# Kernel optimization log

Measured on AMD Instinct MI355X. Metric: run time of the kernel, lower is better.

Reference implementation:

```python
import jax, jax.numpy as jnp
import numpy as np

B, S, DIN, DOUT, A, T, H = 8, 1024, 1024, 1024, 4, 4, 8  # arity A, T cell types, hidden H


def setup_inputs() -> dict:
    key = jax.random.key(0)
    ks = jax.random.split(key, 6)
    x = jax.random.normal(ks[0], (B, S, DIN), jnp.float32)
    sc = 1.0 / np.sqrt(DIN).astype(np.float32)
    weight = jax.random.uniform(ks[1], (A * DOUT, DIN), jnp.float32, -sc, sc)
    bias = jax.random.uniform(ks[2], (A * DOUT,), jnp.float32, -sc, sc)
    # stacked per-cell-type MLP params: arity -> H -> 1 (tanh)
    cw1 = jax.random.normal(ks[3], (T, A, H), jnp.float32) / np.sqrt(A).astype(np.float32)
    cb1 = jnp.zeros((T, H), jnp.float32)
    cw2 = jax.random.normal(ks[4], (T, H), jnp.float32) / np.sqrt(H).astype(np.float32)
    cb2 = jnp.zeros((T,), jnp.float32)
    return {"x": x, "weight": weight, "bias": bias,
            "cw1": cw1, "cb1": cb1, "cw2": cw2, "cb2": cb2}


def reference(x, weight, bias, cw1, cb1, cw2, cb2):
    T_, A_, H_ = cw1.shape
    Dout = weight.shape[0] // A_
    G = Dout // T_  # neurons per cell type (cell_indices = contiguous blocks via np.repeat)
    # all_inputs = F.linear(input, weight, bias): (B, S, A*Dout)
    z = jnp.einsum('bsd,od->bso', x, weight) + bias
    # slice per-neuron arity chunks -> (B, S, T, G, A)
    z = z.reshape(z.shape[0], z.shape[1], T_, G, A_)
    # per-cell-type MLP applied to every neuron of that type (replaces Python loop)
    h = jnp.tanh(jnp.einsum('bstga,tah->bstgh', z, cw1) + cb1[:, None, :])
    o = jnp.einsum('bstgh,th->bstg', h, cw2) + cb2[:, None]
    # concat over neurons -> (B, S, Dout)
    return o.reshape(o.shape[0], o.shape[1], Dout)
```

## Files before the change

### kernel.cpp

```cpp
#include <hip/hip_runtime.h>


typedef __bf16 bf16x8 __attribute__((ext_vector_type(8)));
typedef float f32x4 __attribute__((ext_vector_type(4)));
typedef float f32x16 __attribute__((ext_vector_type(16)));

#define BM 128
#define BN 128
#define BK 32
#define KDIM 1024
#define NITER (KDIM / BK)
#define ABUF_E (BM * BK)
#define BUF_E ((BM + BN) * BK)
#define BUF_BYTES (BUF_E * 2)
#define XN8 (8192 * 1024 / 8)
#define WN8 (4096 * 1024 / 8)

__global__ __launch_bounds__(256) void cvt_bf16_kernel(
    const float* __restrict__ x, const float* __restrict__ w,
    __bf16* __restrict__ xb, __bf16* __restrict__ wb) {
    int i = blockIdx.x * 256 + threadIdx.x;
    const float* src;
    __bf16* dst;
    int j;
    if (i < XN8) { src = x; dst = xb; j = i; }
    else         { src = w; dst = wb; j = i - XN8; }
    const f32x4* p = (const f32x4*)src + 2 * (size_t)j;
    f32x4 a = p[0], b = p[1];
    bf16x8 o;
    o[0] = (__bf16)a[0]; o[1] = (__bf16)a[1]; o[2] = (__bf16)a[2]; o[3] = (__bf16)a[3];
    o[4] = (__bf16)b[0]; o[5] = (__bf16)b[1]; o[6] = (__bf16)b[2]; o[7] = (__bf16)b[3];
    ((bf16x8*)dst)[j] = o;
}

union __align__(16) SmemU {
    __bf16 stg[2 * BUF_E];
    float  z[64 * 128];
};

__global__ __launch_bounds__(256, 4) void fused_gemm_mlp_kernel(
    const __bf16* __restrict__ Ag,
    const __bf16* __restrict__ Bg,
    const float* __restrict__ bias,
    const float* __restrict__ cw1,
    const float* __restrict__ cb1,
    const float* __restrict__ cw2,
    const float* __restrict__ cb2,
    float* __restrict__ out)
{
    __shared__ SmemU u;

    const int tid  = threadIdx.x;
    const int wave = tid >> 6;
    const int lane = tid & 63;
    const int wm = wave >> 1;
    const int wn = wave & 1;
    const int bn0 = blockIdx.x * BN;
    const int bm0 = blockIdx.y * BM;

    f32x16 acc[2][2] = {};

    const int srow4 = lane >> 2;
    const int g8    = (((lane & 3) ^ ((lane >> 3) & 3)) * 8);

    const int lr5 = lane & 31;
    const int lk2 = lane >> 5;
    const int sw2 = (lr5 >> 1) & 3;
    const int arow = (wm * 64 + lr5) * (BK * 2);
    const int brow = ABUF_E * 2 + (wn * 64 + lr5) * (BK * 2);
    int cxo[2];
#pragma unroll
    for (int kh = 0; kh < 2; ++kh)
        cxo[kh] = ((kh * 2 + lk2) ^ sw2) * 16;
    const char* sb = (const char*)u.stg;

    const __bf16* aBase = Ag + (size_t)(bm0 + (wave * 2) * 16 + srow4) * KDIM + g8;
    const __bf16* bBase = Bg + (size_t)(bn0 + (wave * 2) * 16 + srow4) * KDIM + g8;

    auto stage = [&](int it, int buf) {
        __bf16* dstA = u.stg + buf * BUF_E;
        __bf16* dstB = dstA + ABUF_E;
        const int kof = it * BK;
#pragma unroll
        for (int c = 0; c < 2; ++c) {
            const int chunk = wave * 2 + c;
            __builtin_amdgcn_global_load_lds(
                (__attribute__((address_space(1))) void*)(aBase + (size_t)c * 16 * KDIM + kof),
                (__attribute__((address_space(3))) void*)&dstA[chunk * 512],
                16, 0, 0);
            __builtin_amdgcn_global_load_lds(
                (__attribute__((address_space(1))) void*)(bBase + (size_t)c * 16 * KDIM + kof),
                (__attribute__((address_space(3))) void*)&dstB[chunk * 512],
                16, 0, 0);
        }
    };

    stage(0, 0);
    for (int it = 0; it < NITER; ++it) {
        __syncthreads();
        if (it + 1 < NITER) stage(it + 1, (it + 1) & 1);
        const char* base = sb + (it & 1) * BUF_BYTES;
#pragma unroll
        for (int kh = 0; kh < 2; ++kh) {
            bf16x8 af[2], bfr[2];
#pragma unroll
            for (int mi = 0; mi < 2; ++mi)
                af[mi] = *(const bf16x8*)(base + arow + mi * 2048 + cxo[kh]);
#pragma unroll
            for (int ni = 0; ni < 2; ++ni)
                bfr[ni] = *(const bf16x8*)(base + brow + ni * 2048 + cxo[kh]);
#pragma unroll
            for (int mi = 0; mi < 2; ++mi)
#pragma unroll
                for (int ni = 0; ni < 2; ++ni)
                    acc[mi][ni] = __builtin_amdgcn_mfma_f32_32x32x16_bf16(
                        af[mi], bfr[ni], acc[mi][ni], 0, 0, 0);
        }
    }
    __syncthreads();

    const int t = bn0 >> 10;
    const float L2E2 = 2.885390081777927f;
    float oinit = cb2[t];
#pragma unroll
    for (int i = 0; i < 8; ++i) oinit += cw2[t * 8 + i];

    float bcol[2];
#pragma unroll
    for (int ni = 0; ni < 2; ++ni)
        bcol[ni] = bias[bn0 + wn * 64 + ni * 32 + lr5];

#pragma unroll
    for (int h = 0; h < 2; ++h) {
        if (wm == h) {
#pragma unroll
            for (int mi = 0; mi < 2; ++mi) {
#pragma unroll
                for (int ni = 0; ni < 2; ++ni) {
                    const int n  = wn * 64 + ni * 32 + lr5;
                    const int gc = n >> 2;
                    const int a  = n & 3;
#pragma unroll
                    for (int g = 0; g < 4; ++g) {
                        const int rb = mi * 32 + g * 8 + lk2 * 4;
#pragma unroll
                        for (int j = 0; j < 4; ++j) {
                            const int chunk = (gc + j) & 31;
                            u.z[(rb + j) * 128 + chunk * 4 + a] =
                                acc[mi][ni][g * 4 + j] + bcol[ni];
                        }
                    }
                }
            }
        }
        __syncthreads();

#pragma unroll
        for (int it2 = 0; it2 < 8; ++it2) {
            const int i = tid + it2 * 256;
            const int q = (i & 7) + 8 * ((i >> 8) & 3);
            const int r = ((i >> 3) & 31) + 32 * (i >> 10);
            const int chunk = (q + (r & 3)) & 31;
            f32x4 z = *(const f32x4*)&u.z[r * 128 + chunk * 4];
            float o = oinit;
#pragma unroll
            for (int hh = 0; hh < 8; ++hh) {
                float pre = z[0] * cw1[t * 32 + 0 * 8 + hh] + z[1] * cw1[t * 32 + 1 * 8 + hh]
                          + z[2] * cw1[t * 32 + 2 * 8 + hh] + z[3] * cw1[t * 32 + 3 * 8 + hh]
                          + cb1[t * 8 + hh];
                float e = __builtin_amdgcn_exp2f(pre * L2E2);
                o -= 2.0f * cw2[t * 8 + hh] * __builtin_amdgcn_rcpf(e + 1.0f);
            }
            out[(size_t)(bm0 + h * 64 + r) * 1024 + (bn0 >> 2) + q] = o;
        }
        __syncthreads();
    }
}

extern "C" void kernel_launch(void* const* d_in, const int* in_sizes, int n_in,
                              void* d_out, int out_size, void* d_ws, size_t ws_size,
                              hipStream_t stream) {
    const float* x    = (const float*)d_in[0];
    const float* w    = (const float*)d_in[1];
    const float* bias = (const float*)d_in[2];
    const float* cw1  = (const float*)d_in[3];
    const float* cb1  = (const float*)d_in[4];
    const float* cw2  = (const float*)d_in[5];
    const float* cb2  = (const float*)d_in[6];
    float* out = (float*)d_out;

    __bf16* xb = (__bf16*)d_ws;
    __bf16* wb = xb + (size_t)8192 * 1024;

    cvt_bf16_kernel<<<(XN8 + WN8) / 256, 256, 0, stream>>>(x, w, xb, wb);

    dim3 grid(4096 / BN, 8192 / BM);
    fused_gemm_mlp_kernel<<<grid, 256, 0, stream>>>(xb, wb, bias, cw1, cb1, cw2, cb2, out);
}
```

Before: 200.9 us.

## Pack weight into MFMA-fragment layout and load B directly to registers

The conversion kernel now writes the bf16 weight in a k8-major packed layout, so each lane can load its B fragment straight from global memory into registers. This bypasses LDS staging for B. Only A is staged through LDS, and the main loop is unrolled by two with explicit register double-buffering of B. The __launch_bounds__ occupancy hint of 4 is dropped. B now comes from global/L2 with no LDS reuse, which may raise global traffic and latency exposure, and register pressure goes up with the two B buffers.

```diff
diff --git a/kernel.cpp b/kernel.cpp
--- a/kernel.cpp
+++ b/kernel.cpp
@@ -9,38 +9,44 @@
 #define BN 128
 #define BK 32
 #define KDIM 1024
+#define NDIM 4096
 #define NITER (KDIM / BK)
-#define ABUF_E (BM * BK)
-#define BUF_E ((BM + BN) * BK)
-#define BUF_BYTES (BUF_E * 2)
+#define ABUF_B 8192
 #define XN8 (8192 * 1024 / 8)
 #define WN8 (4096 * 1024 / 8)
 
-__global__ __launch_bounds__(256) void cvt_bf16_kernel(
+__global__ __launch_bounds__(256) void cvt_pack_kernel(
     const float* __restrict__ x, const float* __restrict__ w,
-    __bf16* __restrict__ xb, __bf16* __restrict__ wb) {
+    __bf16* __restrict__ xb, __bf16* __restrict__ wbp) {
     int i = blockIdx.x * 256 + threadIdx.x;
-    const float* src;
-    __bf16* dst;
-    int j;
-    if (i < XN8) { src = x; dst = xb; j = i; }
-    else         { src = w; dst = wb; j = i - XN8; }
-    const f32x4* p = (const f32x4*)src + 2 * (size_t)j;
-    f32x4 a = p[0], b = p[1];
-    bf16x8 o;
-    o[0] = (__bf16)a[0]; o[1] = (__bf16)a[1]; o[2] = (__bf16)a[2]; o[3] = (__bf16)a[3];
-    o[4] = (__bf16)b[0]; o[5] = (__bf16)b[1]; o[6] = (__bf16)b[2]; o[7] = (__bf16)b[3];
-    ((bf16x8*)dst)[j] = o;
+    if (i < XN8) {
+        const f32x4* p = (const f32x4*)x + 2 * (size_t)i;
+        f32x4 a = p[0], b = p[1];
+        bf16x8 o;
+        o[0]=(__bf16)a[0]; o[1]=(__bf16)a[1]; o[2]=(__bf16)a[2]; o[3]=(__bf16)a[3];
+        o[4]=(__bf16)b[0]; o[5]=(__bf16)b[1]; o[6]=(__bf16)b[2]; o[7]=(__bf16)b[3];
+        ((bf16x8*)xb)[i] = o;
+    } else {
+        const int j  = i - XN8;
+        const int n  = j >> 7;
+        const int k8 = j & 127;
+        const f32x4* p = (const f32x4*)(w + (size_t)n * KDIM + k8 * 8);
+        f32x4 a = p[0], b = p[1];
+        bf16x8 o;
+        o[0]=(__bf16)a[0]; o[1]=(__bf16)a[1]; o[2]=(__bf16)a[2]; o[3]=(__bf16)a[3];
+        o[4]=(__bf16)b[0]; o[5]=(__bf16)b[1]; o[6]=(__bf16)b[2]; o[7]=(__bf16)b[3];
+        ((bf16x8*)wbp)[(size_t)k8 * NDIM + n] = o;
+    }
 }
 
 union __align__(16) SmemU {
-    __bf16 stg[2 * BUF_E];
+    __bf16 stg[2 * (ABUF_B / 2)];
     float  z[64 * 128];
 };
 
-__global__ __launch_bounds__(256, 4) void fused_gemm_mlp_kernel(
+__global__ __launch_bounds__(256) void fused_gemm_mlp_kernel(
     const __bf16* __restrict__ Ag,
-    const __bf16* __restrict__ Bg,
+    const __bf16* __restrict__ Bw,
     const float* __restrict__ bias,
     const float* __restrict__ cw1,
     const float* __restrict__ cb1,
@@ -67,55 +73,69 @@
     const int lk2 = lane >> 5;
     const int sw2 = (lr5 >> 1) & 3;
     const int arow = (wm * 64 + lr5) * (BK * 2);
-    const int brow = ABUF_E * 2 + (wn * 64 + lr5) * (BK * 2);
     int cxo[2];
 #pragma unroll
     for (int kh = 0; kh < 2; ++kh)
         cxo[kh] = ((kh * 2 + lk2) ^ sw2) * 16;
     const char* sb = (const char*)u.stg;
 
-    const __bf16* aBase = Ag + (size_t)(bm0 + (wave * 2) * 16 + srow4) * KDIM + g8;
-    const __bf16* bBase = Bg + (size_t)(bn0 + (wave * 2) * 16 + srow4) * KDIM + g8;
+    const size_t bvoff = ((size_t)lk2 * NDIM + bn0 + wn * 64 + lr5) * 8;
+
+    const __bf16* aBase = Ag + (size_t)(bm0 + wave * 32 + srow4) * KDIM + g8;
 
     auto stage = [&](int it, int buf) {
-        __bf16* dstA = u.stg + buf * BUF_E;
-        __bf16* dstB = dstA + ABUF_E;
+        __bf16* dstA = u.stg + buf * (ABUF_B / 2);
         const int kof = it * BK;
 #pragma unroll
         for (int c = 0; c < 2; ++c) {
-            const int chunk = wave * 2 + c;
             __builtin_amdgcn_global_load_lds(
                 (__attribute__((address_space(1))) void*)(aBase + (size_t)c * 16 * KDIM + kof),
-                (__attribute__((address_space(3))) void*)&dstA[chunk * 512],
+                (__attribute__((address_space(3))) void*)&dstA[(wave * 2 + c) * 512],
                 16, 0, 0);
-            __builtin_amdgcn_global_load_lds(
-                (__attribute__((address_space(1))) void*)(bBase + (size_t)c * 16 * KDIM + kof),
-                (__attribute__((address_space(3))) void*)&dstB[chunk * 512],
-                16, 0, 0);
         }
     };
 
-    stage(0, 0);
-    for (int it = 0; it < NITER; ++it) {
-        __syncthreads();
-        if (it + 1 < NITER) stage(it + 1, (it + 1) & 1);
-        const char* base = sb + (it & 1) * BUF_BYTES;
+    auto loadB = [&](int it, bf16x8 b[2][2]) {
+        const __bf16* bp = Bw + (size_t)it * 4 * NDIM * 8 + bvoff;
+#pragma unroll
+        for (int kh = 0; kh < 2; ++kh)
+#pragma unroll
+            for (int ni = 0; ni < 2; ++ni)
+                b[kh][ni] = *(const bf16x8*)(bp + (size_t)kh * 2 * NDIM * 8 + ni * 32 * 8);
+    };
+
+    auto compute = [&](int buf, const bf16x8 b[2][2]) {
+        const char* base = sb + buf * ABUF_B;
 #pragma unroll
         for (int kh = 0; kh < 2; ++kh) {
-            bf16x8 af[2], bfr[2];
+            bf16x8 af[2];
 #pragma unroll
             for (int mi = 0; mi < 2; ++mi)
                 af[mi] = *(const bf16x8*)(base + arow + mi * 2048 + cxo[kh]);
 #pragma unroll
-            for (int ni = 0; ni < 2; ++ni)
-                bfr[ni] = *(const bf16x8*)(base + brow + ni * 2048 + cxo[kh]);
-#pragma unroll
             for (int mi = 0; mi < 2; ++mi)
 #pragma unroll
                 for (int ni = 0; ni < 2; ++ni)
                     acc[mi][ni] = __builtin_amdgcn_mfma_f32_32x32x16_bf16(
-                        af[mi], bfr[ni], acc[mi][ni], 0, 0, 0);
-        }
+                        af[mi], b[kh][ni], acc[mi][ni], 0, 0, 0);
+        }
+    };
+
+    bf16x8 b0[2][2], b1[2][2];
+    stage(0, 0);
+    loadB(0, b0);
+#pragma unroll 1
+    for (int it = 0; it < NITER; it += 2) {
+        __syncthreads();
+        stage(it + 1, 1);
+        loadB(it + 1, b1);
+        compute(0, b0);
+        __syncthreads();
+        if (it + 2 < NITER) {
+            stage(it + 2, 0);
+            loadB(it + 2, b0);
+        }
+        compute(1, b1);
     }
     __syncthreads();
 
@@ -189,11 +209,11 @@
     const float* cb2  = (const float*)d_in[6];
     float* out = (float*)d_out;
 
-    __bf16* xb = (__bf16*)d_ws;
-    __bf16* wb = xb + (size_t)8192 * 1024;
-
-    cvt_bf16_kernel<<<(XN8 + WN8) / 256, 256, 0, stream>>>(x, w, xb, wb);
+    __bf16* xb  = (__bf16*)d_ws;
+    __bf16* wbp = xb + (size_t)8192 * 1024;
+
+    cvt_pack_kernel<<<(XN8 + WN8) / 256, 256, 0, stream>>>(x, w, xb, wbp);
 
     dim3 grid(4096 / BN, 8192 / BM);
-    fused_gemm_mlp_kernel<<<grid, 256, 0, stream>>>(xb, wb, bias, cw1, cb1, cw2, cb2, out);
+    fused_gemm_mlp_kernel<<<grid, 256, 0, stream>>>(xb, wbp, bias, cw1, cb1, cw2, cb2, out);
 }
```

After: 225.0 us. 1.12x slower.
